# Optimization experiments

Hardware: AMD Instinct MI355X
Metric: run time of the kernel (lower is better)

The kernel has to match this reference:

```python
import jax, jax.numpy as jnp
import numpy as np

COMMITMENT_FACTOR = 0.25
QUANTIZATION_FACTOR = 1.0


def setup_inputs() -> dict:
    key = jax.random.key(0)
    k1, k2 = jax.random.split(key)
    B, D, H, W = 64, 256, 32, 32
    K = 1024
    z = jax.random.normal(k1, (B, D, H, W), dtype=jnp.float32)
    # torch init: uniform(-1/K, 1/K)
    codebook = jax.random.uniform(k2, (K, D), dtype=jnp.float32,
                                  minval=-1.0 / K, maxval=1.0 / K)
    return {"z": z, "codebook": codebook}


def reference(z, codebook):
    # z: [B, D, H, W]; codebook: [K, D]
    B, D, H, W = z.shape
    z_nhwc = jnp.transpose(z, (0, 2, 3, 1))          # [B, H, W, D]
    z_flat = z_nhwc.reshape(-1, D)                    # [N, D]
    # squared euclidean distances: ||z||^2 + ||w||^2 - 2 z.w
    dist = (jnp.sum(z_flat ** 2, axis=-1, keepdims=True)
            + jnp.sum(codebook ** 2, axis=-1)
            - 2.0 * z_flat @ codebook.T)              # [N, K]
    closest = jnp.argmin(dist, axis=-1)               # [N]
    quantized_indices = closest.reshape(B, H, W)
    # one-hot @ codebook == gather
    q_flat = codebook[closest]                        # [N, D]
    quantized = q_flat.reshape(B, H, W, D)

    commitment_loss = jnp.sum((jax.lax.stop_gradient(quantized) - z_nhwc) ** 2)
    embedding_loss = jnp.sum((quantized - jax.lax.stop_gradient(z_nhwc)) ** 2)
    loss = commitment_loss * COMMITMENT_FACTOR + embedding_loss * QUANTIZATION_FACTOR

    # straight-through estimator
    quantized_st = z_nhwc + jax.lax.stop_gradient(quantized - z_nhwc)
    quantized_st = jnp.transpose(quantized_st, (0, 3, 1, 2))  # [B, D, H, W]
    quantized_indices = quantized_indices[:, None, :, :]       # [B, 1, H, W]
    return quantized_st, quantized_indices, loss
```

## Files before the change

### kernel.cpp

```cpp
#include <hip/hip_runtime.h>


#define IDX_OFF  16777216
#define LOSS_OFF 16842752

typedef __bf16 bf16x8 __attribute__((ext_vector_type(8)));
typedef float  f32x4  __attribute__((ext_vector_type(4)));

__global__ __launch_bounds__(256) void vq_prep(const float* __restrict__ cb,
                                               __bf16* __restrict__ cbh,
                                               float* __restrict__ sc1) {
    const int t = threadIdx.x;
    const int r = blockIdx.x * 16 + (t >> 4);
    const int d0 = (t & 15) * 16;
    const float* src = cb + (size_t)r * 256 + d0;
    __bf16* dst = cbh + (size_t)r * 256 + d0;
    float s = 0.f;
    float4 f[4];
    #pragma unroll
    for (int p = 0; p < 4; p++) f[p] = *(const float4*)(src + p * 4);
    bf16x8 v0, v1;
    #pragma unroll
    for (int p = 0; p < 4; p++) {
        s = fmaf(f[p].x, f[p].x, s); s = fmaf(f[p].y, f[p].y, s);
        s = fmaf(f[p].z, f[p].z, s); s = fmaf(f[p].w, f[p].w, s);
    }
    v0[0]=(__bf16)f[0].x; v0[1]=(__bf16)f[0].y; v0[2]=(__bf16)f[0].z; v0[3]=(__bf16)f[0].w;
    v0[4]=(__bf16)f[1].x; v0[5]=(__bf16)f[1].y; v0[6]=(__bf16)f[1].z; v0[7]=(__bf16)f[1].w;
    v1[0]=(__bf16)f[2].x; v1[1]=(__bf16)f[2].y; v1[2]=(__bf16)f[2].z; v1[3]=(__bf16)f[2].w;
    v1[4]=(__bf16)f[3].x; v1[5]=(__bf16)f[3].y; v1[6]=(__bf16)f[3].z; v1[7]=(__bf16)f[3].w;
    *(bf16x8*)dst = v0;
    *(bf16x8*)(dst + 8) = v1;
    s += __shfl_xor(s, 1, 64);
    s += __shfl_xor(s, 2, 64);
    s += __shfl_xor(s, 4, 64);
    s += __shfl_xor(s, 8, 64);
    if ((t & 15) == 0) sc1[r] = s + 1.0f;
}

__global__ __launch_bounds__(256, 2) void vq_mfma(const float* __restrict__ z,
                                                  const __bf16* __restrict__ cbh,
                                                  const float* __restrict__ sc1,
                                                  float* __restrict__ out) {
    __shared__ __align__(16) __bf16 z_s[64 * 256];
    __shared__ float red_s[4];

    const int t    = threadIdx.x;
    const int lane = t & 63;
    const int w    = t >> 6;
    const int m16  = lane & 15;
    const int q4   = lane >> 4;
    const int wc   = w << 5;
    const int blk  = blockIdx.x;
    const int b    = blk >> 4;
    const int hw0  = (blk & 15) << 6;
    const int n0   = blk << 6;
    const int kt0  = (blk & 3) << 8;

    bf16x8 bb[2];
    {
        const __bf16* bp = cbh + (size_t)(kt0 + wc + m16) * 256 + q4 * 8;
        bb[0] = *(const bf16x8*)bp;
        bb[1] = *(const bf16x8*)(bp + 4096);
    }

    float lz = 0.f;
    {
        const int nl   = t & 63;
        const int dseg = t >> 6;
        const float* zp = z + (size_t)(b * 256 + dseg * 64) * 1024 + hw0 + nl;
        #pragma unroll
        for (int p = 0; p < 8; p++) {
            bf16x8 v;
            #pragma unroll
            for (int j = 0; j < 8; j++) {
                float f = zp[(size_t)(p * 8 + j) * 1024];
                lz = fmaf(f, f, lz);
                v[j] = (__bf16)f;
            }
            int gs = (dseg * 8 + p) ^ (nl & 7);
            *(bf16x8*)&z_s[nl * 256 + gs * 8] = v;
        }
    }
    __syncthreads();

    unsigned int best[16];
    #pragma unroll
    for (int i = 0; i < 16; i++) best[i] = 0xFFFFFFFFu;

    #pragma unroll 1
    for (int it = 0; it < 8; it++) {
        const int kt  = (kt0 + (it << 7)) & 1023;
        const int ktn = (kt0 + (((it + 1) & 7) << 7)) & 1023;
        int   kcv[2];
        float sck[2];
        #pragma unroll
        for (int j = 0; j < 2; j++) {
            kcv[j] = kt + wc + j * 16 + m16;
            sck[j] = sc1[kcv[j]];
        }
        const __bf16* bc  = cbh + (size_t)(kt + wc + m16) * 256 + q4 * 8;
        const __bf16* bnx = cbh + (size_t)(ktn + wc + m16) * 256 + q4 * 8;

        f32x4 acc[4][2];
        #pragma unroll
        for (int i = 0; i < 4; i++)
            #pragma unroll
            for (int j = 0; j < 2; j++) acc[i][j] = (f32x4){0.f, 0.f, 0.f, 0.f};

        #pragma unroll
        for (int dc = 0; dc < 256; dc += 32) {
            bf16x8 bn[2];
            const __bf16* bp = (dc == 224) ? bnx : (bc + dc + 32);
            bn[0] = *(const bf16x8*)bp;
            bn[1] = *(const bf16x8*)(bp + 4096);

            bf16x8 a[4];
            const int gs = ((dc >> 3) + q4) ^ (m16 & 7);
            #pragma unroll
            for (int i = 0; i < 4; i++)
                a[i] = *(const bf16x8*)&z_s[(i * 16 + m16) * 256 + gs * 8];

            #pragma unroll
            for (int i = 0; i < 4; i++)
                #pragma unroll
                for (int j = 0; j < 2; j++)
                    acc[i][j] = __builtin_amdgcn_mfma_f32_16x16x32_bf16(a[i], bb[j], acc[i][j], 0, 0, 0);

            bb[0] = bn[0];
            bb[1] = bn[1];
        }

        #pragma unroll
        for (int j = 0; j < 2; j++) {
            #pragma unroll
            for (int i = 0; i < 4; i++)
                #pragma unroll
                for (int r = 0; r < 4; r++) {
                    float v3 = fmaf(-2.f, acc[i][j][r], sck[j]);
                    unsigned int key = (__float_as_uint(v3) & 0xFFFFFC00u) | (unsigned int)kcv[j];
                    int pos = i * 4 + r;
                    best[pos] = min(best[pos], key);
                }
        }
    }

    #pragma unroll
    for (int pos = 0; pos < 16; pos++) {
        unsigned int k = best[pos];
        #pragma unroll
        for (int off = 1; off < 16; off <<= 1)
            k = min(k, (unsigned int)__shfl_xor((int)k, off, 64));
        best[pos] = k;
    }
    __syncthreads();

    unsigned int* ks = (unsigned int*)z_s;
    if (m16 == 0) {
        #pragma unroll
        for (int pos = 0; pos < 16; pos++) {
            int i = pos >> 2, r = pos & 3;
            int row = i * 16 + q4 * 4 + r;
            ks[w * 64 + row] = best[pos];
        }
    }
    __syncthreads();
    if (t < 64) {
        unsigned int key = min(min(ks[t], ks[64 + t]), min(ks[128 + t], ks[192 + t]));
        int kf = (int)(key & 1023u);
        ks[256 + t] = (unsigned int)kf;
        out[IDX_OFF + n0 + t] = (float)kf;
        lz += __uint_as_float(key & 0xFFFFFC00u) - 1.0f;
    }
    {
        float s = lz;
        #pragma unroll
        for (int off = 1; off < 64; off <<= 1) s += __shfl_xor(s, off, 64);
        if (lane == 0) red_s[w] = s;
    }
    __syncthreads();
    if (t == 0)
        atomicAdd(out + LOSS_OFF, 1.25f * ((red_s[0] + red_s[1]) + (red_s[2] + red_s[3])));

    const int qrow = t >> 2;
    const int qoff = (t & 3) * 64;
    const int myk  = (int)ks[256 + qrow];
    __syncthreads();
    {
        const __bf16* qp = cbh + (size_t)myk * 256 + qoff;
        #pragma unroll
        for (int p = 0; p < 8; p++) {
            bf16x8 v = *(const bf16x8*)(qp + p * 8);
            int gs = ((qoff >> 3) + p) ^ (qrow & 7);
            *(bf16x8*)&z_s[qrow * 256 + gs * 8] = v;
        }
    }
    __syncthreads();
    {
        const int nl   = t & 63;
        const int dseg = t >> 6;
        float* op = out + (size_t)(b * 256 + dseg * 64) * 1024 + hw0 + nl;
        #pragma unroll
        for (int p = 0; p < 8; p++) {
            int gs = (dseg * 8 + p) ^ (nl & 7);
            bf16x8 v = *(const bf16x8*)&z_s[nl * 256 + gs * 8];
            #pragma unroll
            for (int j = 0; j < 8; j++)
                op[(size_t)(p * 8 + j) * 1024] = (float)v[j];
        }
    }
}

extern "C" void kernel_launch(void* const* d_in, const int* in_sizes, int n_in,
                              void* d_out, int out_size, void* d_ws, size_t ws_size,
                              hipStream_t stream) {
    const float* z  = (const float*)d_in[0];
    const float* cb = (const float*)d_in[1];
    float* out = (float*)d_out;

    float*  sc1 = (float*)d_ws;
    __bf16* cbh = (__bf16*)((char*)d_ws + 8192);

    hipMemsetAsync(out + LOSS_OFF, 0, sizeof(float), stream);
    vq_prep<<<64, 256, 0, stream>>>(cb, cbh, sc1);
    vq_mfma<<<1024, 256, 0, stream>>>(z, cbh, sc1, out);
}
```

Baseline: 181.7 us.

## Deepen codebook prefetch to two stages, prefetch LDS A-fragments, vectorize z loads

The codebook B-fragment register prefetch goes from one to two k-steps ahead, and the LDS A-fragments for the next k-step are loaded before the current MFMAs are issued. Both changes aim to hide global and LDS latency behind the matrix instructions. The z staging loads switch from scalar strided reads to float4 reads covering four spatial positions per thread, which cuts the number of load instructions. In exchange, register pressure rises, which may hurt under the two-blocks-per-SM launch bound.

```diff
diff --git a/kernel.cpp b/kernel.cpp
--- a/kernel.cpp
+++ b/kernel.cpp
@@ -57,29 +57,40 @@
     const int n0   = blk << 6;
     const int kt0  = (blk & 3) << 8;
 
-    bf16x8 bb[2];
+    bf16x8 bb0[2], bb1[2];
     {
         const __bf16* bp = cbh + (size_t)(kt0 + wc + m16) * 256 + q4 * 8;
-        bb[0] = *(const bf16x8*)bp;
-        bb[1] = *(const bf16x8*)(bp + 4096);
+        bb0[0] = *(const bf16x8*)bp;
+        bb0[1] = *(const bf16x8*)(bp + 4096);
+        bb1[0] = *(const bf16x8*)(bp + 32);
+        bb1[1] = *(const bf16x8*)(bp + 32 + 4096);
     }
 
     float lz = 0.f;
     {
-        const int nl   = t & 63;
-        const int dseg = t >> 6;
-        const float* zp = z + (size_t)(b * 256 + dseg * 64) * 1024 + hw0 + nl;
-        #pragma unroll
-        for (int p = 0; p < 8; p++) {
-            bf16x8 v;
-            #pragma unroll
-            for (int j = 0; j < 8; j++) {
-                float f = zp[(size_t)(p * 8 + j) * 1024];
-                lz = fmaf(f, f, lz);
-                v[j] = (__bf16)f;
+        const int rg    = (t & 15) * 4;
+        const int dbase = (t >> 4) * 16;
+        const float* zp = z + (size_t)b * 262144 + hw0 + rg;
+        #pragma unroll
+        for (int batch = 0; batch < 2; batch++) {
+            float4 f[8];
+            #pragma unroll
+            for (int j = 0; j < 8; j++)
+                f[j] = *(const float4*)(zp + (size_t)(dbase + batch * 8 + j) * 1024);
+            const float* fp = (const float*)f;
+            #pragma unroll
+            for (int r = 0; r < 4; r++) {
+                bf16x8 v;
+                #pragma unroll
+                for (int j = 0; j < 8; j++) {
+                    float x = fp[j * 4 + r];
+                    lz = fmaf(x, x, lz);
+                    v[j] = (__bf16)x;
+                }
+                const int row = rg + r;
+                const int gs  = ((t >> 4) * 2 + batch) ^ (row & 7);
+                *(bf16x8*)&z_s[row * 256 + gs * 8] = v;
             }
-            int gs = (dseg * 8 + p) ^ (nl & 7);
-            *(bf16x8*)&z_s[nl * 256 + gs * 8] = v;
         }
     }
     __syncthreads();
@@ -87,6 +98,14 @@
     unsigned int best[16];
     #pragma unroll
     for (int i = 0; i < 16; i++) best[i] = 0xFFFFFFFFu;
+
+    bf16x8 a0[4];
+    {
+        const int gs = q4 ^ (m16 & 7);
+        #pragma unroll
+        for (int i = 0; i < 4; i++)
+            a0[i] = *(const bf16x8*)&z_s[(i * 16 + m16) * 256 + gs * 8];
+    }
 
     #pragma unroll 1
     for (int it = 0; it < 8; it++) {
@@ -109,26 +128,31 @@
             for (int j = 0; j < 2; j++) acc[i][j] = (f32x4){0.f, 0.f, 0.f, 0.f};
 
         #pragma unroll
-        for (int dc = 0; dc < 256; dc += 32) {
+        for (int dcs = 0; dcs < 8; dcs++) {
+            const int dc = dcs * 32;
             bf16x8 bn[2];
-            const __bf16* bp = (dc == 224) ? bnx : (bc + dc + 32);
+            const __bf16* bp = (dcs < 6) ? (bc + dc + 64) : (bnx + (dc - 192));
             bn[0] = *(const bf16x8*)bp;
             bn[1] = *(const bf16x8*)(bp + 4096);
 
-            bf16x8 a[4];
-            const int gs = ((dc >> 3) + q4) ^ (m16 & 7);
+            bf16x8 an[4];
+            {
+                const int gs = ((((dc + 32) & 255) >> 3) + q4) ^ (m16 & 7);
+                #pragma unroll
+                for (int i = 0; i < 4; i++)
+                    an[i] = *(const bf16x8*)&z_s[(i * 16 + m16) * 256 + gs * 8];
+            }
+
             #pragma unroll
             for (int i = 0; i < 4; i++)
-                a[i] = *(const bf16x8*)&z_s[(i * 16 + m16) * 256 + gs * 8];
-
-            #pragma unroll
-            for (int i = 0; i < 4; i++)
                 #pragma unroll
                 for (int j = 0; j < 2; j++)
-                    acc[i][j] = __builtin_amdgcn_mfma_f32_16x16x32_bf16(a[i], bb[j], acc[i][j], 0, 0, 0);
-
-            bb[0] = bn[0];
-            bb[1] = bn[1];
+                    acc[i][j] = __builtin_amdgcn_mfma_f32_16x16x32_bf16(a0[i], bb0[j], acc[i][j], 0, 0, 0);
+
+            #pragma unroll
+            for (int i = 0; i < 4; i++) a0[i] = an[i];
+            bb0[0] = bb1[0]; bb0[1] = bb1[1];
+            bb1[0] = bn[0];  bb1[1] = bn[1];
         }
 
         #pragma unroll
```

New measurement: 181.2 us. About the same (-0.2%).

## Double rows per block to 128 and vectorize z staging loads

Applied to the files above, without the earlier changes.

Each block now handles 128 z rows instead of 64, with 512 blocks and 64KB of LDS, so every codebook fragment loaded from global/L2 feeds twice as many MFMAs. Loading z into LDS now uses float4 reads along the spatial dimension with an in-register transpose, replacing scalar strided loads. The costs are higher register pressure from 16 accumulators and 32 best keys, possible loss of the 2-blocks-per-CU occupancy, and fewer blocks to spread over the CUs.

```diff
diff --git a/kernel.cpp b/kernel.cpp
--- a/kernel.cpp
+++ b/kernel.cpp
@@ -42,7 +42,7 @@
                                                   const __bf16* __restrict__ cbh,
                                                   const float* __restrict__ sc1,
                                                   float* __restrict__ out) {
-    __shared__ __align__(16) __bf16 z_s[64 * 256];
+    __shared__ __align__(16) __bf16 z_s[128 * 256];
     __shared__ float red_s[4];
 
     const int t    = threadIdx.x;
@@ -52,10 +52,10 @@
     const int q4   = lane >> 4;
     const int wc   = w << 5;
     const int blk  = blockIdx.x;
-    const int b    = blk >> 4;
-    const int hw0  = (blk & 15) << 6;
-    const int n0   = blk << 6;
-    const int kt0  = (blk & 3) << 8;
+    const int b    = blk >> 3;
+    const int hw0  = (blk & 7) << 7;
+    const int n0   = blk << 7;
+    const int kt0  = (blk & 7) << 7;
 
     bf16x8 bb[2];
     {
@@ -66,27 +66,36 @@
 
     float lz = 0.f;
     {
-        const int nl   = t & 63;
-        const int dseg = t >> 6;
-        const float* zp = z + (size_t)(b * 256 + dseg * 64) * 1024 + hw0 + nl;
-        #pragma unroll
-        for (int p = 0; p < 8; p++) {
-            bf16x8 v;
-            #pragma unroll
-            for (int j = 0; j < 8; j++) {
-                float f = zp[(size_t)(p * 8 + j) * 1024];
-                lz = fmaf(f, f, lz);
-                v[j] = (__bf16)f;
+        const int rg    = (t & 31) * 4;
+        const int dbase = (t >> 5) * 32;
+        const float* zp = z + (size_t)b * 262144 + hw0 + rg;
+        #pragma unroll
+        for (int batch = 0; batch < 4; batch++) {
+            float4 f[8];
+            #pragma unroll
+            for (int j = 0; j < 8; j++)
+                f[j] = *(const float4*)(zp + (size_t)(dbase + batch * 8 + j) * 1024);
+            const float* fp = (const float*)f;
+            #pragma unroll
+            for (int r = 0; r < 4; r++) {
+                bf16x8 v;
+                #pragma unroll
+                for (int j = 0; j < 8; j++) {
+                    float x = fp[j * 4 + r];
+                    lz = fmaf(x, x, lz);
+                    v[j] = (__bf16)x;
+                }
+                const int row = rg + r;
+                const int gs  = ((dbase >> 3) + batch) ^ (row & 7);
+                *(bf16x8*)&z_s[row * 256 + gs * 8] = v;
             }
-            int gs = (dseg * 8 + p) ^ (nl & 7);
-            *(bf16x8*)&z_s[nl * 256 + gs * 8] = v;
-        }
-    }
-    __syncthreads();
-
-    unsigned int best[16];
-    #pragma unroll
-    for (int i = 0; i < 16; i++) best[i] = 0xFFFFFFFFu;
+        }
+    }
+    __syncthreads();
+
+    unsigned int best[32];
+    #pragma unroll
+    for (int i = 0; i < 32; i++) best[i] = 0xFFFFFFFFu;
 
     #pragma unroll 1
     for (int it = 0; it < 8; it++) {
@@ -102,30 +111,27 @@
         const __bf16* bc  = cbh + (size_t)(kt + wc + m16) * 256 + q4 * 8;
         const __bf16* bnx = cbh + (size_t)(ktn + wc + m16) * 256 + q4 * 8;
 
-        f32x4 acc[4][2];
-        #pragma unroll
-        for (int i = 0; i < 4; i++)
+        f32x4 acc[8][2];
+        #pragma unroll
+        for (int i = 0; i < 8; i++)
             #pragma unroll
             for (int j = 0; j < 2; j++) acc[i][j] = (f32x4){0.f, 0.f, 0.f, 0.f};
 
         #pragma unroll
-        for (int dc = 0; dc < 256; dc += 32) {
+        for (int dcs = 0; dcs < 8; dcs++) {
+            const int dc = dcs * 32;
             bf16x8 bn[2];
-            const __bf16* bp = (dc == 224) ? bnx : (bc + dc + 32);
+            const __bf16* bp = (dcs < 7) ? (bc + dc + 32) : bnx;
             bn[0] = *(const bf16x8*)bp;
             bn[1] = *(const bf16x8*)(bp + 4096);
 
-            bf16x8 a[4];
             const int gs = ((dc >> 3) + q4) ^ (m16 & 7);
             #pragma unroll
-            for (int i = 0; i < 4; i++)
-                a[i] = *(const bf16x8*)&z_s[(i * 16 + m16) * 256 + gs * 8];
-
-            #pragma unroll
-            for (int i = 0; i < 4; i++)
-                #pragma unroll
-                for (int j = 0; j < 2; j++)
-                    acc[i][j] = __builtin_amdgcn_mfma_f32_16x16x32_bf16(a[i], bb[j], acc[i][j], 0, 0, 0);
+            for (int i = 0; i < 8; i++) {
+                bf16x8 a = *(const bf16x8*)&z_s[(i * 16 + m16) * 256 + gs * 8];
+                acc[i][0] = __builtin_amdgcn_mfma_f32_16x16x32_bf16(a, bb[0], acc[i][0], 0, 0, 0);
+                acc[i][1] = __builtin_amdgcn_mfma_f32_16x16x32_bf16(a, bb[1], acc[i][1], 0, 0, 0);
+            }
 
             bb[0] = bn[0];
             bb[1] = bn[1];
@@ -134,7 +140,7 @@
         #pragma unroll
         for (int j = 0; j < 2; j++) {
             #pragma unroll
-            for (int i = 0; i < 4; i++)
+            for (int i = 0; i < 8; i++)
                 #pragma unroll
                 for (int r = 0; r < 4; r++) {
                     float v3 = fmaf(-2.f, acc[i][j][r], sck[j]);
@@ -146,7 +152,7 @@
     }
 
     #pragma unroll
-    for (int pos = 0; pos < 16; pos++) {
+    for (int pos = 0; pos < 32; pos++) {
         unsigned int k = best[pos];
         #pragma unroll
         for (int off = 1; off < 16; off <<= 1)
@@ -158,17 +164,17 @@
     unsigned int* ks = (unsigned int*)z_s;
     if (m16 == 0) {
         #pragma unroll
-        for (int pos = 0; pos < 16; pos++) {
+        for (int pos = 0; pos < 32; pos++) {
             int i = pos >> 2, r = pos & 3;
             int row = i * 16 + q4 * 4 + r;
-            ks[w * 64 + row] = best[pos];
-        }
-    }
-    __syncthreads();
-    if (t < 64) {
-        unsigned int key = min(min(ks[t], ks[64 + t]), min(ks[128 + t], ks[192 + t]));
+            ks[w * 128 + row] = best[pos];
+        }
+    }
+    __syncthreads();
+    if (t < 128) {
+        unsigned int key = min(min(ks[t], ks[128 + t]), min(ks[256 + t], ks[384 + t]));
         int kf = (int)(key & 1023u);
-        ks[256 + t] = (unsigned int)kf;
+        ks[512 + t] = (unsigned int)kf;
         out[IDX_OFF + n0 + t] = (float)kf;
         lz += __uint_as_float(key & 0xFFFFFC00u) - 1.0f;
     }
@@ -182,14 +188,14 @@
     if (t == 0)
         atomicAdd(out + LOSS_OFF, 1.25f * ((red_s[0] + red_s[1]) + (red_s[2] + red_s[3])));
 
-    const int qrow = t >> 2;
-    const int qoff = (t & 3) * 64;
-    const int myk  = (int)ks[256 + qrow];
+    const int qrow = t >> 1;
+    const int qoff = (t & 1) * 128;
+    const int myk  = (int)ks[512 + qrow];
     __syncthreads();
     {
         const __bf16* qp = cbh + (size_t)myk * 256 + qoff;
         #pragma unroll
-        for (int p = 0; p < 8; p++) {
+        for (int p = 0; p < 16; p++) {
             bf16x8 v = *(const bf16x8*)(qp + p * 8);
             int gs = ((qoff >> 3) + p) ^ (qrow & 7);
             *(bf16x8*)&z_s[qrow * 256 + gs * 8] = v;
@@ -197,12 +203,12 @@
     }
     __syncthreads();
     {
-        const int nl   = t & 63;
-        const int dseg = t >> 6;
-        float* op = out + (size_t)(b * 256 + dseg * 64) * 1024 + hw0 + nl;
-        #pragma unroll
-        for (int p = 0; p < 8; p++) {
-            int gs = (dseg * 8 + p) ^ (nl & 7);
+        const int nl   = t & 127;
+        const int dseg = t >> 7;
+        float* op = out + (size_t)(b * 256 + dseg * 128) * 1024 + hw0 + nl;
+        #pragma unroll
+        for (int p = 0; p < 16; p++) {
+            int gs = (dseg * 16 + p) ^ (nl & 7);
             bf16x8 v = *(const bf16x8*)&z_s[nl * 256 + gs * 8];
             #pragma unroll
             for (int j = 0; j < 8; j++)
@@ -223,5 +229,5 @@
 
     hipMemsetAsync(out + LOSS_OFF, 0, sizeof(float), stream);
     vq_prep<<<64, 256, 0, stream>>>(cb, cbh, sc1);
-    vq_mfma<<<1024, 256, 0, stream>>>(z, cbh, sc1, out);
+    vq_mfma<<<512, 256, 0, stream>>>(z, cbh, sc1, out);
 }
```

Result: slower. 249.6 us (+37.4%).
